# Optimization experiments

Hardware: AMD Instinct MI355X
Metric: run time of the kernel (lower is better)

The kernel has to match this reference:

```python
import jax, jax.numpy as jnp
import numpy as np

B, C, H, W = 8, 256, 128, 128
N = H * W
TEMP = 0.07
NUM_NEG = 128
HARD_RADIUS = 4
HARD_RATIO = 0.75   # curriculum fully ramped (_current_hard_ratio == hard_ratio_max)
N_HARD = int(NUM_NEG * HARD_RATIO)   # 96
N_RAND = NUM_NEG - N_HARD            # 32
STEP = max(1, H // 16)               # 8
N_POS = ((H + STEP - 1) // STEP) * ((W + STEP - 1) // STEP)  # 256


def setup_inputs() -> dict:
    key = jax.random.key(0)
    ks = jax.random.split(key, 8)
    fmap_rgb = jax.random.normal(ks[0], (B, C, H, W), jnp.float32)
    fmap_depth = jax.random.normal(ks[1], (B, C, H, W), jnp.float32)
    pu = jax.random.uniform(ks[2], (B, H, W), jnp.float32) * (W - 1)
    pv = jax.random.uniform(ks[3], (B, H, W), jnp.float32) * (H - 1)
    projected_coords = jnp.stack([pu, pv], axis=1)  # (B,2,H,W)
    valid_mask = (jax.random.uniform(ks[4], (B, H, W)) < 0.9).astype(jnp.float32)
    rand_idx = jax.random.randint(ks[5], (B, N_RAND), 0, N, dtype=jnp.int32)
    hard_off_u = jax.random.randint(ks[6], (B, N_HARD, N_POS), -HARD_RADIUS, HARD_RADIUS + 1, dtype=jnp.int32)
    hard_off_v = jax.random.randint(ks[7], (B, N_HARD, N_POS), -HARD_RADIUS, HARD_RADIUS + 1, dtype=jnp.int32)
    return {
        'fmap_rgb': fmap_rgb, 'fmap_depth': fmap_depth,
        'projected_coords': projected_coords, 'valid_mask': valid_mask,
        'rand_idx': rand_idx, 'hard_off_u': hard_off_u, 'hard_off_v': hard_off_v,
    }


def _normalize(x):
    # F.normalize(dim=1): x / max(||x||_2, eps)
    n = jnp.sqrt(jnp.sum(x * x, axis=1, keepdims=True))
    return x / jnp.maximum(n, 1e-12)


def _bilinear_sample(f, x, y):
    # grid_sample(mode=bilinear, padding=zeros, align_corners=True); unnormalized
    # coords equal pixel coords (x=proj_u, y=proj_v). f:(B,C,H,W), x,y:(B,H,W) -> (B,C,N)
    Bb, Cc, Hh, Ww = f.shape
    ff = f.reshape(Bb, Cc, Hh * Ww)
    xf = x.reshape(Bb, -1)
    yf = y.reshape(Bb, -1)
    x0 = jnp.floor(xf)
    y0 = jnp.floor(yf)
    wx = xf - x0
    wy = yf - y0
    x0i = x0.astype(jnp.int32)
    y0i = y0.astype(jnp.int32)

    def g(ix, iy):
        valid = (ix >= 0) & (ix < Ww) & (iy >= 0) & (iy < Hh)
        idx = jnp.clip(iy, 0, Hh - 1) * Ww + jnp.clip(ix, 0, Ww - 1)
        v = jnp.take_along_axis(ff, idx[:, None, :], axis=2)
        return v * valid[:, None, :]

    return (((1 - wx) * (1 - wy))[:, None, :] * g(x0i, y0i)
            + (wx * (1 - wy))[:, None, :] * g(x0i + 1, y0i)
            + ((1 - wx) * wy)[:, None, :] * g(x0i, y0i + 1)
            + (wx * wy)[:, None, :] * g(x0i + 1, y0i + 1))


def reference(fmap_rgb, fmap_depth, projected_coords, valid_mask, rand_idx, hard_off_u, hard_off_v):
    rgb = _normalize(fmap_rgb)
    dep = _normalize(fmap_depth)
    proj_u = projected_coords[:, 0]
    proj_v = projected_coords[:, 1]

    rgb_pos = _bilinear_sample(rgb, proj_u, proj_v)        # (B,C,N)
    dep_flat = dep.reshape(B, C, N)
    rgb_flat = rgb.reshape(B, C, N)
    pos_sim = jnp.sum(dep_flat * rgb_pos, axis=1) / TEMP    # (B,N)

    # random negatives via gather + batched matmul
    rgb_rand = jnp.take_along_axis(rgb_flat, rand_idx[:, None, :].astype(jnp.int32), axis=2)  # (B,C,n_rand)
    rand_neg = jnp.einsum('bcn,bck->bkn', dep_flat, rgb_rand) / TEMP  # (B,n_rand,N)

    # hard negatives on coarse grid (step = H//16)
    gh = jnp.arange(0, H, STEP)
    gw = jnp.arange(0, W, STEP)
    ghf, gwf = [a.reshape(-1) for a in jnp.meshgrid(gh, gw, indexing='ij')]
    grid_idx = ghf * W + gwf                                # (n_pos,)
    pos_u = jnp.clip(proj_u[:, ghf, gwf], 0, W - 1).astype(jnp.int32)  # (B,n_pos)
    pos_v = jnp.clip(proj_v[:, ghf, gwf], 0, H - 1).astype(jnp.int32)
    off_u = jnp.where((hard_off_u == 0) & (hard_off_v == 0), 1, hard_off_u)
    hu = jnp.clip(pos_u[:, None, :] + off_u, 0, W - 1)      # (B,n_hard,n_pos)
    hv = jnp.clip(pos_v[:, None, :] + hard_off_v, 0, H - 1)
    hard_idx = (hv * W + hu).reshape(B, -1)                 # (B, n_hard*n_pos)
    rgb_hard = jnp.take_along_axis(rgb_flat, hard_idx[:, None, :], axis=2).reshape(B, C, N_HARD, N_POS)
    dep_grid = dep_flat[:, :, grid_idx]                     # (B,C,n_pos)
    hard_sim = jnp.einsum('bcp,bchp->bhp', dep_grid, rgb_hard) / TEMP  # (B,n_hard,n_pos)

    # logsumexp over [pos; random negs; hard negs] -- hard negs only exist at grid
    # positions (the torch code scatters into a dense -inf (B,n_hard,N) tensor;
    # logaddexp at grid positions is mathematically identical and avoids it).
    lse_base = jax.scipy.special.logsumexp(
        jnp.concatenate([pos_sim[:, None, :], rand_neg], axis=1), axis=1)  # (B,N)
    lse_hard = jax.scipy.special.logsumexp(hard_sim, axis=1)               # (B,n_pos)
    lse = lse_base.at[:, grid_idx].set(jnp.logaddexp(lse_base[:, grid_idx], lse_hard))

    mask = valid_mask.reshape(B, N)
    denom = jnp.maximum(jnp.sum(mask), 1.0)
    loss = jnp.sum((lse - pos_sim) * mask) / denom

    # accuracy (no_grad in torch); max over all negatives, hard ones only at grid idx
    max_neg = jnp.max(rand_neg, axis=1)
    max_neg = max_neg.at[:, grid_idx].max(jnp.max(hard_sim, axis=1))
    correct = ((pos_sim > max_neg) & (mask > 0.5)).astype(jnp.float32)
    accuracy = jnp.sum(correct) / denom * 100.0
    return loss, jax.lax.stop_gradient(accuracy)
```

## Files before the change

### kernel.cpp

```cpp
#include <hip/hip_runtime.h>
#include <cfloat>
#include <math.h>

#define B_ 8
#define C_ 256
#define C2_ (C_/2)
#define H_ 128
#define W_ 128
#define N_ (H_*W_)
#define NRAND 32
#define NHARD 96
#define NPOS 256
#define INV_TEMP (1.0f/0.07f)

__device__ __forceinline__ unsigned bf16rne(float x) {
    unsigned u = __float_as_uint(x);
    return (u + 0x7FFFu + ((u >> 16) & 1u)) >> 16;
}
__device__ __forceinline__ float blo(unsigned w) { return __uint_as_float(w << 16); }
__device__ __forceinline__ float bhi(unsigned w) { return __uint_as_float(w & 0xFFFF0000u); }

__global__ __launch_bounds__(256) void k1_rgb_norm_T(const float* __restrict__ rgb,
                                                     unsigned* __restrict__ rgbT) {
    __shared__ float tile[C_][67];
    __shared__ float redx[8][32], redy[8][32];
    __shared__ float invn[64];
    int bi = blockIdx.x;
    int b  = bi >> 8;
    int p0 = (bi & 255) << 6;
    int t  = threadIdx.x;
    int pxh = t & 31;
    int cg  = t >> 5;
    const float2* src2 = (const float2*)(rgb + (size_t)b * C_ * N_);
    float ssx = 0.f, ssy = 0.f;
    #pragma unroll 4
    for (int p = 0; p < 32; ++p) {
        int c = p * 8 + cg;
        float2 v = src2[(size_t)c * (N_ / 2) + (p0 >> 1) + pxh];
        tile[c][2 * pxh]     = v.x;
        tile[c][2 * pxh + 1] = v.y;
        ssx += v.x * v.x;
        ssy += v.y * v.y;
    }
    redx[cg][pxh] = ssx; redy[cg][pxh] = ssy;
    __syncthreads();
    if (t < 32) {
        float sx = 0.f, sy = 0.f;
        #pragma unroll
        for (int g2 = 0; g2 < 8; ++g2) { sx += redx[g2][t]; sy += redy[g2][t]; }
        invn[2 * t]     = 1.0f / fmaxf(sqrtf(sx), 1e-12f);
        invn[2 * t + 1] = 1.0f / fmaxf(sqrtf(sy), 1e-12f);
    }
    __syncthreads();
    unsigned* dst = rgbT + (size_t)(b * N_ + p0) * C2_;
    int u  = t & 127;
    int ph = t >> 7;
    #pragma unroll 4
    for (int it = 0; it < 32; ++it) {
        int px = ph + 2 * it;
        float sc = invn[px];
        unsigned pa = bf16rne(tile[2 * u][px] * sc);
        unsigned pb = bf16rne(tile[2 * u + 1][px] * sc);
        dst[(size_t)px * C2_ + u] = pa | (pb << 16);
    }
}

__global__ __launch_bounds__(256) void k2_main(
        const float* __restrict__ dep, const unsigned* __restrict__ rgbT,
        const float* __restrict__ coords, const int* __restrict__ rand_idx,
        float* __restrict__ lse_base, float* __restrict__ pos_out,
        float* __restrict__ maxneg_out) {
    __shared__ float dep_lds[64][64];
    __shared__ __align__(16) float rand_lds[32][256];
    __shared__ float red[4][64];
    __shared__ float invn[64];
    int bi = blockIdx.x;
    int b  = bi >> 8;
    int p0 = (bi & 255) << 6;
    int t  = threadIdx.x;
    {
        int u  = t & 127, kh = t >> 7;
        #pragma unroll 4
        for (int pass = 0; pass < 16; ++pass) {
            int k = kh + 2 * pass;
            int idx = rand_idx[b * NRAND + k];
            unsigned w = rgbT[(size_t)(b * N_ + idx) * C2_ + u];
            rand_lds[k][2 * u]     = blo(w);
            rand_lds[k][2 * u + 1] = bhi(w);
        }
    }
    int px = t >> 2, g = t & 3;
    int n  = p0 + px;
    float xf = coords[(size_t)b * 2 * N_ + n];
    float yf = coords[(size_t)b * 2 * N_ + N_ + n];
    float x0 = floorf(xf), y0 = floorf(yf);
    float wx = xf - x0, wy = yf - y0;
    int ix = (int)x0 + (g & 1);
    int iy = (int)y0 + (g >> 1);
    float wgt = ((g & 1) ? wx : 1.f - wx) * ((g & 2) ? wy : 1.f - wy);
    if (ix < 0 || ix >= W_ || iy < 0 || iy >= H_) wgt = 0.f;
    int ixc = min(max(ix, 0), W_ - 1), iyc = min(max(iy, 0), H_ - 1);
    const unsigned* nbr = rgbT + (size_t)(b * N_ + iyc * W_ + ixc) * C2_;
    const float* depb = dep + (size_t)b * C_ * N_;
    float accN = 0.f, accR[8];
    #pragma unroll
    for (int j = 0; j < 8; ++j) accR[j] = 0.f;
    float ss = 0.f;
    int lane = t & 63, w = t >> 6;
    __syncthreads();
    for (int ch = 0; ch < 4; ++ch) {
        #pragma unroll
        for (int i = 0; i < 16; ++i) {
            int cc = w * 16 + i;
            float v = depb[(size_t)(ch * 64 + cc) * N_ + p0 + lane];
            dep_lds[cc][lane] = v;
            ss += v * v;
        }
        if (ch == 3) red[w][lane] = ss;
        __syncthreads();
        #pragma unroll
        for (int c4i = 0; c4i < 16; ++c4i) {
            int c4 = (c4i + 2 * g) & 15;
            int cc = c4 * 4;
            int c  = ch * 64 + cc;
            float d0 = dep_lds[cc + 0][px];
            float d1 = dep_lds[cc + 1][px];
            float d2 = dep_lds[cc + 2][px];
            float d3 = dep_lds[cc + 3][px];
            uint2 q = *(const uint2*)(nbr + (c >> 1));
            accN += d0 * blo(q.x) + d1 * bhi(q.x) + d2 * blo(q.y) + d3 * bhi(q.y);
            #pragma unroll
            for (int j = 0; j < 8; ++j) {
                const float4 r = *(const float4*)(&rand_lds[g * 8 + j][c]);
                accR[j] += d0 * r.x + d1 * r.y + d2 * r.z + d3 * r.w;
            }
        }
        __syncthreads();
    }
    if (t < 64) {
        float s = red[0][t] + red[1][t] + red[2][t] + red[3][t];
        invn[t] = 1.0f / fmaxf(sqrtf(s), 1e-12f);
    }
    __syncthreads();
    float scale = invn[px] * INV_TEMP;
    float pp = accN * wgt;
    pp += __shfl_xor(pp, 1, 4);
    pp += __shfl_xor(pp, 2, 4);
    float pos = pp * scale;
    float r[8];
    float ml = -FLT_MAX;
    #pragma unroll
    for (int j = 0; j < 8; ++j) { r[j] = accR[j] * scale; ml = fmaxf(ml, r[j]); }
    ml = fmaxf(ml, __shfl_xor(ml, 1, 4));
    ml = fmaxf(ml, __shfl_xor(ml, 2, 4));
    float mneg = ml;
    float mall = fmaxf(mneg, pos);
    float se = 0.f;
    #pragma unroll
    for (int j = 0; j < 8; ++j) se += expf(r[j] - mall);
    se += __shfl_xor(se, 1, 4);
    se += __shfl_xor(se, 2, 4);
    if (g == 0) {
        float lse = mall + logf(se + expf(pos - mall));
        size_t o = (size_t)b * N_ + n;
        lse_base[o]   = lse;
        pos_out[o]    = pos;
        maxneg_out[o] = mneg;
    }
}

__global__ __launch_bounds__(128) void k3_hard(
        const float* __restrict__ dep, const unsigned* __restrict__ rgbT,
        const float* __restrict__ coords, const int* __restrict__ hoffu,
        const int* __restrict__ hoffv, float* __restrict__ lse_hard,
        float* __restrict__ max_hard) {
    __shared__ __align__(16) float dv[256];
    __shared__ float sred[2], sm_[2], ss_[2];
    int bp = blockIdx.x;
    int b = bp >> 8, p = bp & 255;
    int gy = (p >> 4) * 8, gx = (p & 15) * 8;
    int n  = gy * W_ + gx;
    int t  = threadIdx.x;
    const float* depb = dep + (size_t)b * C_ * N_;
    float v0 = depb[(size_t)t * N_ + n];
    float v1 = depb[(size_t)(t + 128) * N_ + n];
    dv[t] = v0; dv[t + 128] = v1;
    float ssq = v0 * v0 + v1 * v1;
    #pragma unroll
    for (int o = 32; o > 0; o >>= 1) ssq += __shfl_down(ssq, o, 64);
    int wid = t >> 6;
    if ((t & 63) == 0) sred[wid] = ssq;
    __syncthreads();
    float inv_n = 1.0f / fmaxf(sqrtf(sred[0] + sred[1]), 1e-12f);
    float pu = coords[(size_t)b * 2 * N_ + n];
    float pv = coords[(size_t)b * 2 * N_ + N_ + n];
    int iu = (int)fminf(fmaxf(pu, 0.f), (float)(W_ - 1));
    int iv = (int)fminf(fmaxf(pv, 0.f), (float)(H_ - 1));
    float sim = -FLT_MAX;
    if (t < NHARD) {
        int ou = hoffu[((size_t)b * NHARD + t) * NPOS + p];
        int ov = hoffv[((size_t)b * NHARD + t) * NPOS + p];
        if (ou == 0 && ov == 0) ou = 1;
        int hu = min(max(iu + ou, 0), W_ - 1);
        int hv = min(max(iv + ov, 0), H_ - 1);
        const uint4* hvec = (const uint4*)(rgbT + (size_t)(b * N_ + hv * W_ + hu) * C2_);
        float acc = 0.f;
        #pragma unroll 4
        for (int c8 = 0; c8 < 32; ++c8) {
            uint4 q = hvec[c8];
            float4 d0 = *(const float4*)(&dv[c8 * 8]);
            float4 d1 = *(const float4*)(&dv[c8 * 8 + 4]);
            acc += d0.x * blo(q.x) + d0.y * bhi(q.x)
                 + d0.z * blo(q.y) + d0.w * bhi(q.y)
                 + d1.x * blo(q.z) + d1.y * bhi(q.z)
                 + d1.z * blo(q.w) + d1.w * bhi(q.w);
        }
        sim = acc * inv_n * INV_TEMP;
    }
    float m = sim;
    #pragma unroll
    for (int o = 32; o > 0; o >>= 1) m = fmaxf(m, __shfl_down(m, o, 64));
    if ((t & 63) == 0) sm_[wid] = m;
    __syncthreads();
    float mm = fmaxf(sm_[0], sm_[1]);
    float e = (t < NHARD) ? expf(sim - mm) : 0.f;
    #pragma unroll
    for (int o = 32; o > 0; o >>= 1) e += __shfl_down(e, o, 64);
    if ((t & 63) == 0) ss_[wid] = e;
    __syncthreads();
    if (t == 0) {
        lse_hard[bp] = mm + logf(ss_[0] + ss_[1]);
        max_hard[bp] = mm;
    }
}

__global__ __launch_bounds__(256) void k4_reduce(
        const float* __restrict__ lse_base, const float* __restrict__ pos_sim,
        const float* __restrict__ max_neg, const float* __restrict__ mask,
        const float* __restrict__ lse_hard, const float* __restrict__ max_hard,
        float* __restrict__ acc) {
    int i = blockIdx.x * 256 + threadIdx.x;
    float l  = lse_base[i], ps = pos_sim[i], mn = max_neg[i], mk = mask[i];
    int b = i >> 14;
    int n = i & (N_ - 1);
    int y = n >> 7, x = n & 127;
    if (((y & 7) | (x & 7)) == 0) {
        int p = ((y >> 3) << 4) + (x >> 3);
        float lh = lse_hard[(b << 8) + p];
        float mh = max_hard[(b << 8) + p];
        float m = fmaxf(l, lh);
        l  = m + logf(expf(l - m) + expf(lh - m));
        mn = fmaxf(mn, mh);
    }
    float s0 = (l - ps) * mk;
    float s1 = (ps > mn && mk > 0.5f) ? 1.f : 0.f;
    float s2 = mk;
    #pragma unroll
    for (int o = 32; o > 0; o >>= 1) {
        s0 += __shfl_down(s0, o, 64);
        s1 += __shfl_down(s1, o, 64);
        s2 += __shfl_down(s2, o, 64);
    }
    __shared__ float r0[4], r1[4], r2[4];
    int wid = threadIdx.x >> 6;
    if ((threadIdx.x & 63) == 0) { r0[wid] = s0; r1[wid] = s1; r2[wid] = s2; }
    __syncthreads();
    if (threadIdx.x == 0) {
        atomicAdd(&acc[0], r0[0] + r0[1] + r0[2] + r0[3]);
        atomicAdd(&acc[1], r1[0] + r1[1] + r1[2] + r1[3]);
        atomicAdd(&acc[2], r2[0] + r2[1] + r2[2] + r2[3]);
    }
}

__global__ void k5_final(const float* __restrict__ acc, float* __restrict__ out) {
    if (threadIdx.x == 0) {
        float denom = fmaxf(acc[2], 1.0f);
        out[0] = acc[0] / denom;
        out[1] = acc[1] / denom * 100.0f;
    }
}

extern "C" void kernel_launch(void* const* d_in, const int* in_sizes, int n_in,
                              void* d_out, int out_size, void* d_ws, size_t ws_size,
                              hipStream_t stream) {
    const float* rgb     = (const float*)d_in[0];
    const float* dep     = (const float*)d_in[1];
    const float* coords  = (const float*)d_in[2];
    const float* mask    = (const float*)d_in[3];
    const int*   rand_i  = (const int*)d_in[4];
    const int*   hoffu   = (const int*)d_in[5];
    const int*   hoffv   = (const int*)d_in[6];
    float* out = (float*)d_out;
    char*  ws  = (char*)d_ws;

    const size_t RGBT_B = (size_t)B_ * N_ * C_ * 2;
    const size_t PIX_B  = (size_t)B_ * N_ * 4;
    unsigned* rgbT  = (unsigned*)ws;
    float* lse_base = (float*)(ws + RGBT_B);
    float* pos_sim  = (float*)(ws + RGBT_B + PIX_B);
    float* max_neg  = (float*)(ws + RGBT_B + 2 * PIX_B);
    float* lse_hard = (float*)(ws + RGBT_B + 3 * PIX_B);
    float* max_hard = (float*)(ws + RGBT_B + 3 * PIX_B + 8192);
    float* acc      = (float*)(ws + RGBT_B + 3 * PIX_B + 2 * 8192);

    hipMemsetAsync(acc, 0, 16, stream);
    k1_rgb_norm_T<<<B_ * (N_ / 64), 256, 0, stream>>>(rgb, rgbT);
    k2_main<<<B_ * (N_ / 64), 256, 0, stream>>>(dep, rgbT, coords, rand_i,
                                                lse_base, pos_sim, max_neg);
    k3_hard<<<B_ * NPOS, 128, 0, stream>>>(dep, rgbT, coords, hoffu, hoffv,
                                           lse_hard, max_hard);
    k4_reduce<<<(B_ * N_) / 256, 256, 0, stream>>>(lse_base, pos_sim, max_neg,
                                                   mask, lse_hard, max_hard, acc);
    k5_final<<<1, 64, 0, stream>>>(acc, out);
}
```

Baseline: 414.4 us.

## Use bf16 MFMA for random-negative sims and pass normalized grid depth to hard kernel

k2 now loads the whole 256-channel depth tile once, converts it to bf16 in swizzled LDS, and computes the 64x32 random-negative similarity block with 16x16x32 bf16 MFMA instead of scalar FMAs over fp32 LDS. The positive dot product is read from the same bf16 LDS tile. k2 also writes normalized bf16 depth vectors for grid pixels to a workspace buffer, so k3 no longer re-gathers strided depth channels or recomputes norms. This adds bf16 rounding of the depth features, which changes numerics slightly.

```diff
diff --git a/kernel.cpp b/kernel.cpp
--- a/kernel.cpp
+++ b/kernel.cpp
@@ -12,6 +12,9 @@
 #define NHARD 96
 #define NPOS 256
 #define INV_TEMP (1.0f/0.07f)
+
+typedef __attribute__((ext_vector_type(8))) short short8;
+typedef __attribute__((ext_vector_type(4))) float f32x4;
 
 __device__ __forceinline__ unsigned bf16rne(float x) {
     unsigned u = __float_as_uint(x);
@@ -69,26 +72,47 @@
         const float* __restrict__ dep, const unsigned* __restrict__ rgbT,
         const float* __restrict__ coords, const int* __restrict__ rand_idx,
         float* __restrict__ lse_base, float* __restrict__ pos_out,
-        float* __restrict__ maxneg_out) {
-    __shared__ float dep_lds[64][64];
-    __shared__ __align__(16) float rand_lds[32][256];
+        float* __restrict__ maxneg_out, unsigned* __restrict__ depG) {
+    __shared__ __align__(16) uint4 dep4[64 * 32];
+    __shared__ __align__(16) uint4 rs4[32 * 32];
     __shared__ float red[4][64];
     __shared__ float invn[64];
     int bi = blockIdx.x;
     int b  = bi >> 8;
     int p0 = (bi & 255) << 6;
     int t  = threadIdx.x;
-    {
-        int u  = t & 127, kh = t >> 7;
-        #pragma unroll 4
-        for (int pass = 0; pass < 16; ++pass) {
-            int k = kh + 2 * pass;
-            int idx = rand_idx[b * NRAND + k];
-            unsigned w = rgbT[(size_t)(b * N_ + idx) * C2_ + u];
-            rand_lds[k][2 * u]     = blo(w);
-            rand_lds[k][2 * u + 1] = bhi(w);
+    int lane = t & 63, w = t >> 6;
+
+    #pragma unroll
+    for (int it = 0; it < 4; ++it) {
+        int flat = it * 256 + t;
+        int rn = flat >> 5, c8 = flat & 31;
+        int idx = rand_idx[b * NRAND + rn];
+        const uint4* src = (const uint4*)(rgbT + (size_t)(b * N_ + idx) * C2_);
+        rs4[rn * 32 + (c8 ^ (rn & 7))] = src[c8];
+    }
+
+    const float* depb = dep + (size_t)b * C_ * N_ + p0 + lane;
+    float ssq = 0.f;
+    int psw = lane & 7;
+    #pragma unroll 2
+    for (int i = 0; i < 8; ++i) {
+        int c0 = w * 64 + i * 8;
+        float v[8];
+        #pragma unroll
+        for (int k = 0; k < 8; ++k) {
+            v[k] = depb[(size_t)(c0 + k) * N_];
+            ssq += v[k] * v[k];
         }
-    }
+        uint4 q;
+        q.x = bf16rne(v[0]) | (bf16rne(v[1]) << 16);
+        q.y = bf16rne(v[2]) | (bf16rne(v[3]) << 16);
+        q.z = bf16rne(v[4]) | (bf16rne(v[5]) << 16);
+        q.w = bf16rne(v[6]) | (bf16rne(v[7]) << 16);
+        dep4[lane * 32 + ((w * 8 + i) ^ psw)] = q;
+    }
+    red[w][lane] = ssq;
+
     int px = t >> 2, g = t & 3;
     int n  = p0 + px;
     float xf = coords[(size_t)b * 2 * N_ + n];
@@ -100,57 +124,67 @@
     float wgt = ((g & 1) ? wx : 1.f - wx) * ((g & 2) ? wy : 1.f - wy);
     if (ix < 0 || ix >= W_ || iy < 0 || iy >= H_) wgt = 0.f;
     int ixc = min(max(ix, 0), W_ - 1), iyc = min(max(iy, 0), H_ - 1);
-    const unsigned* nbr = rgbT + (size_t)(b * N_ + iyc * W_ + ixc) * C2_;
-    const float* depb = dep + (size_t)b * C_ * N_;
-    float accN = 0.f, accR[8];
-    #pragma unroll
-    for (int j = 0; j < 8; ++j) accR[j] = 0.f;
-    float ss = 0.f;
-    int lane = t & 63, w = t >> 6;
-    __syncthreads();
-    for (int ch = 0; ch < 4; ++ch) {
-        #pragma unroll
-        for (int i = 0; i < 16; ++i) {
-            int cc = w * 16 + i;
-            float v = depb[(size_t)(ch * 64 + cc) * N_ + p0 + lane];
-            dep_lds[cc][lane] = v;
-            ss += v * v;
-        }
-        if (ch == 3) red[w][lane] = ss;
-        __syncthreads();
-        #pragma unroll
-        for (int c4i = 0; c4i < 16; ++c4i) {
-            int c4 = (c4i + 2 * g) & 15;
-            int cc = c4 * 4;
-            int c  = ch * 64 + cc;
-            float d0 = dep_lds[cc + 0][px];
-            float d1 = dep_lds[cc + 1][px];
-            float d2 = dep_lds[cc + 2][px];
-            float d3 = dep_lds[cc + 3][px];
-            uint2 q = *(const uint2*)(nbr + (c >> 1));
-            accN += d0 * blo(q.x) + d1 * bhi(q.x) + d2 * blo(q.y) + d3 * bhi(q.y);
-            #pragma unroll
-            for (int j = 0; j < 8; ++j) {
-                const float4 r = *(const float4*)(&rand_lds[g * 8 + j][c]);
-                accR[j] += d0 * r.x + d1 * r.y + d2 * r.z + d3 * r.w;
-            }
-        }
-        __syncthreads();
-    }
+    const uint4* nbr4 = (const uint4*)(rgbT + (size_t)(b * N_ + iyc * W_ + ixc) * C2_);
+
+    __syncthreads();
     if (t < 64) {
         float s = red[0][t] + red[1][t] + red[2][t] + red[3][t];
         invn[t] = 1.0f / fmaxf(sqrtf(s), 1e-12f);
     }
-    __syncthreads();
+
+    f32x4 acc0 = {0.f, 0.f, 0.f, 0.f};
+    f32x4 acc1 = {0.f, 0.f, 0.f, 0.f};
+    int l15 = lane & 15, l4 = lane >> 4;
+    int pxA = (w << 4) + l15;
+    const short8* lds8 = (const short8*)dep4;
+    const short8* rnd8 = (const short8*)rs4;
+    #pragma unroll
+    for (int kc = 0; kc < 8; ++kc) {
+        int c8 = kc * 4 + l4;
+        short8 a  = lds8[pxA * 32 + (c8 ^ (pxA & 7))];
+        short8 b0 = rnd8[l15 * 32 + (c8 ^ (l15 & 7))];
+        short8 b1 = rnd8[(16 + l15) * 32 + (c8 ^ (l15 & 7))];
+        acc0 = __builtin_amdgcn_mfma_f32_16x16x32_bf16(a, b0, acc0, 0, 0, 0);
+        acc1 = __builtin_amdgcn_mfma_f32_16x16x32_bf16(a, b1, acc1, 0, 0, 0);
+    }
+
+    float accN = 0.f;
+    const uint4* drow = dep4 + (size_t)px * 32;
+    int dsw = px & 7;
+    #pragma unroll 4
+    for (int c8 = 0; c8 < 32; ++c8) {
+        uint4 dq = drow[c8 ^ dsw];
+        uint4 rq = nbr4[c8];
+        accN += blo(dq.x) * blo(rq.x) + bhi(dq.x) * bhi(rq.x)
+              + blo(dq.y) * blo(rq.y) + bhi(dq.y) * bhi(rq.y)
+              + blo(dq.z) * blo(rq.z) + bhi(dq.z) * bhi(rq.z)
+              + blo(dq.w) * blo(rq.w) + bhi(dq.w) * bhi(rq.w);
+    }
+    __syncthreads();
+
+    float* simsF = (float*)rs4;
+    #pragma unroll
+    for (int r = 0; r < 4; ++r) {
+        int prow = (w << 4) + (l4 << 2) + r;
+        int swn = r << 2;
+        simsF[prow * 32 + (l15 ^ swn)]        = acc0[r];
+        simsF[prow * 32 + (16 + (l15 ^ swn))] = acc1[r];
+    }
+    __syncthreads();
+
     float scale = invn[px] * INV_TEMP;
     float pp = accN * wgt;
     pp += __shfl_xor(pp, 1, 4);
     pp += __shfl_xor(pp, 2, 4);
     float pos = pp * scale;
-    float r[8];
+    const float4* sf = (const float4*)simsF;
+    int fsw = px & 3;
+    float4 ra = sf[px * 8 + ((g * 2) ^ fsw)];
+    float4 rb = sf[px * 8 + (((g * 2) ^ fsw) ^ 1)];
+    float r[8] = {ra.x, ra.y, ra.z, ra.w, rb.x, rb.y, rb.z, rb.w};
     float ml = -FLT_MAX;
     #pragma unroll
-    for (int j = 0; j < 8; ++j) { r[j] = accR[j] * scale; ml = fmaxf(ml, r[j]); }
+    for (int j = 0; j < 8; ++j) { r[j] *= scale; ml = fmaxf(ml, r[j]); }
     ml = fmaxf(ml, __shfl_xor(ml, 1, 4));
     ml = fmaxf(ml, __shfl_xor(ml, 2, 4));
     float mneg = ml;
@@ -167,39 +201,53 @@
         pos_out[o]    = pos;
         maxneg_out[o] = mneg;
     }
+
+    int y = p0 >> 7;
+    if ((y & 7) == 0) {
+        int m = t >> 5, u = t & 31;
+        int gpx = m * 8;
+        int gx  = (p0 & 127) + gpx;
+        int p   = ((y >> 3) << 4) + (gx >> 3);
+        float sc = invn[gpx];
+        const unsigned* srow = (const unsigned*)(dep4 + (size_t)gpx * 32);
+        int xsw = (gpx & 7) << 2;
+        unsigned* dst = depG + (size_t)((b << 8) + p) * 128;
+        #pragma unroll
+        for (int it = 0; it < 4; ++it) {
+            int uu = u + it * 32;
+            unsigned wv = srow[uu ^ xsw];
+            dst[uu] = bf16rne(blo(wv) * sc) | (bf16rne(bhi(wv) * sc) << 16);
+        }
+    }
 }
 
 __global__ __launch_bounds__(128) void k3_hard(
-        const float* __restrict__ dep, const unsigned* __restrict__ rgbT,
+        const unsigned* __restrict__ depG, const unsigned* __restrict__ rgbT,
         const float* __restrict__ coords, const int* __restrict__ hoffu,
         const int* __restrict__ hoffv, float* __restrict__ lse_hard,
         float* __restrict__ max_hard) {
     __shared__ __align__(16) float dv[256];
-    __shared__ float sred[2], sm_[2], ss_[2];
+    __shared__ float sm_[2], ss_[2];
     int bp = blockIdx.x;
     int b = bp >> 8, p = bp & 255;
     int gy = (p >> 4) * 8, gx = (p & 15) * 8;
-    int n  = gy * W_ + gx;
+    int nn = gy * W_ + gx;
     int t  = threadIdx.x;
-    const float* depb = dep + (size_t)b * C_ * N_;
-    float v0 = depb[(size_t)t * N_ + n];
-    float v1 = depb[(size_t)(t + 128) * N_ + n];
-    dv[t] = v0; dv[t + 128] = v1;
-    float ssq = v0 * v0 + v1 * v1;
-    #pragma unroll
-    for (int o = 32; o > 0; o >>= 1) ssq += __shfl_down(ssq, o, 64);
-    int wid = t >> 6;
-    if ((t & 63) == 0) sred[wid] = ssq;
-    __syncthreads();
-    float inv_n = 1.0f / fmaxf(sqrtf(sred[0] + sred[1]), 1e-12f);
-    float pu = coords[(size_t)b * 2 * N_ + n];
-    float pv = coords[(size_t)b * 2 * N_ + N_ + n];
+    unsigned wv = depG[(size_t)bp * 128 + t];
+    dv[2 * t]     = blo(wv);
+    dv[2 * t + 1] = bhi(wv);
+    float pu = coords[(size_t)b * 2 * N_ + nn];
+    float pv = coords[(size_t)b * 2 * N_ + N_ + nn];
     int iu = (int)fminf(fmaxf(pu, 0.f), (float)(W_ - 1));
     int iv = (int)fminf(fmaxf(pv, 0.f), (float)(H_ - 1));
     float sim = -FLT_MAX;
+    int ou = 0, ov = 0;
     if (t < NHARD) {
-        int ou = hoffu[((size_t)b * NHARD + t) * NPOS + p];
-        int ov = hoffv[((size_t)b * NHARD + t) * NPOS + p];
+        ou = hoffu[((size_t)b * NHARD + t) * NPOS + p];
+        ov = hoffv[((size_t)b * NHARD + t) * NPOS + p];
+    }
+    __syncthreads();
+    if (t < NHARD) {
         if (ou == 0 && ov == 0) ou = 1;
         int hu = min(max(iu + ou, 0), W_ - 1);
         int hv = min(max(iv + ov, 0), H_ - 1);
@@ -215,11 +263,12 @@
                  + d1.x * blo(q.z) + d1.y * bhi(q.z)
                  + d1.z * blo(q.w) + d1.w * bhi(q.w);
         }
-        sim = acc * inv_n * INV_TEMP;
+        sim = acc * INV_TEMP;
     }
     float m = sim;
     #pragma unroll
     for (int o = 32; o > 0; o >>= 1) m = fmaxf(m, __shfl_down(m, o, 64));
+    int wid = t >> 6;
     if ((t & 63) == 0) sm_[wid] = m;
     __syncthreads();
     float mm = fmaxf(sm_[0], sm_[1]);
@@ -302,12 +351,13 @@
     float* lse_hard = (float*)(ws + RGBT_B + 3 * PIX_B);
     float* max_hard = (float*)(ws + RGBT_B + 3 * PIX_B + 8192);
     float* acc      = (float*)(ws + RGBT_B + 3 * PIX_B + 2 * 8192);
+    unsigned* depG  = (unsigned*)(ws + RGBT_B + 3 * PIX_B + 2 * 8192 + 1024);
 
     hipMemsetAsync(acc, 0, 16, stream);
     k1_rgb_norm_T<<<B_ * (N_ / 64), 256, 0, stream>>>(rgb, rgbT);
     k2_main<<<B_ * (N_ / 64), 256, 0, stream>>>(dep, rgbT, coords, rand_i,
-                                                lse_base, pos_sim, max_neg);
-    k3_hard<<<B_ * NPOS, 128, 0, stream>>>(dep, rgbT, coords, hoffu, hoffv,
+                                                lse_base, pos_sim, max_neg, depG);
+    k3_hard<<<B_ * NPOS, 128, 0, stream>>>(depG, rgbT, coords, hoffu, hoffv,
                                            lse_hard, max_hard);
     k4_reduce<<<(B_ * N_) / 256, 256, 0, stream>>>(lse_base, pos_sim, max_neg,
                                                    mask, lse_hard, max_hard, acc);
```

New measurement: 370.4 us. 10.6% less time.
